# Performance work log

Hardware: AMD Instinct MI355X
Metric: run time of the kernel (lower is better)

The kernel has to match this reference:

```python
import jax, jax.numpy as jnp
import numpy as np

HEADS = 20  # head_dim = 1280 // 20 = 64
LORA_SCALE = 1.0


def setup_inputs() -> dict:
    key = jax.random.key(0)
    ks = jax.random.split(key, 16)
    B, S, C, R = 2, 2048, 1280, 4
    w = 0.02  # keep activations numerically tame
    inp = {
        "x": jax.random.normal(ks[0], (B, S, C), jnp.float32),
        "Wq": jax.random.normal(ks[1], (C, C), jnp.float32) * w,
        "Wk": jax.random.normal(ks[2], (C, C), jnp.float32) * w,
        "Wv": jax.random.normal(ks[3], (C, C), jnp.float32) * w,
        "Wo": jax.random.normal(ks[4], (C, C), jnp.float32) * w,
        "bo": jnp.zeros((C,), jnp.float32),
        "Aq": jax.random.normal(ks[5], (R, C), jnp.float32) * w,
        "Bq": jax.random.normal(ks[6], (C, R), jnp.float32) * w,
        "Ak": jax.random.normal(ks[7], (R, C), jnp.float32) * w,
        "Bk": jax.random.normal(ks[8], (C, R), jnp.float32) * w,
        "Av": jax.random.normal(ks[9], (R, C), jnp.float32) * w,
        "Bv": jax.random.normal(ks[10], (C, R), jnp.float32) * w,
        "Ao": jax.random.normal(ks[11], (R, C), jnp.float32) * w,
        "Bo": jax.random.normal(ks[12], (C, R), jnp.float32) * w,
    }
    return inp


def _lora(x, A, B):
    # LoRALinearLayer: up(down(x)); network_alpha=None -> no extra scaling
    return (x @ A.T) @ B.T


def reference(x, Wq, Wk, Wv, Wo, bo, Aq, Bq, Ak, Bk, Av, Bv, Ao, Bo):
    B, S, C = x.shape
    H = HEADS
    D = C // H
    # base projections + LoRA updates (self-attention: encoder_hidden_states = x)
    q = x @ Wq.T + LORA_SCALE * _lora(x, Aq, Bq)
    k = x @ Wk.T + LORA_SCALE * _lora(x, Ak, Bk)
    v = x @ Wv.T + LORA_SCALE * _lora(x, Av, Bv)
    # head split: [B, S, H, D]
    q = q.reshape(B, S, H, D)
    k = k.reshape(B, S, H, D)
    v = v.reshape(B, S, H, D)
    # explicit scores + softmax (attn.get_attention_scores), scale = 1/sqrt(D)
    scale = 1.0 / jnp.sqrt(jnp.asarray(D, x.dtype))
    scores = jnp.einsum("bshd,bthd->bhst", q, k) * scale  # [B, H, S, S]
    probs = jax.nn.softmax(scores, axis=-1)
    ctx = jnp.einsum("bhst,bthd->bshd", probs, v).reshape(B, S, C)
    # output projection (+bias) + LoRA; dropout is identity at eval
    out = ctx @ Wo.T + bo + LORA_SCALE * _lora(ctx, Ao, Bo)
    return out
```

## Files before the change

kernel.cpp:

```cpp
#include <hip/hip_runtime.h>

#define BATCH 2
#define SEQ   2048
#define CH    1280
#define NH    20
#define HD    64
#define BS    (BATCH*SEQ)
#define RK    4

typedef __attribute__((ext_vector_type(2)))  float floatx2;
typedef __attribute__((ext_vector_type(4)))  short bf16x4;
typedef __attribute__((ext_vector_type(8)))  short bf16x8;
typedef __attribute__((ext_vector_type(16))) float floatx16;

__device__ __forceinline__ floatx16 mfma32(bf16x8 a, bf16x8 b, floatx16 c) {
    return __builtin_amdgcn_mfma_f32_32x32x16_bf16(a, b, c, 0, 0, 0);
}

__device__ __forceinline__ unsigned short f2bf(float f) {
    unsigned int u = __float_as_uint(f);
    u += 0x7fffu + ((u >> 16) & 1u);
    return (unsigned short)(u >> 16);
}
__device__ __forceinline__ unsigned int packbf(float hi, float lo) {
    unsigned int a = __float_as_uint(hi) + 0x8000u;
    unsigned int b = __float_as_uint(lo) + 0x8000u;
    return __builtin_amdgcn_perm(a, b, 0x07060302u);
}
__device__ __forceinline__ unsigned int cvtpk(float lo, float hi) {
    unsigned int r;
    asm("v_cvt_pk_bf16_f32 %0, %1, %2" : "=v"(r) : "v"(lo), "v"(hi));
    return r;
}
__device__ __forceinline__ float fexp2(float x) {
#if __has_builtin(__builtin_amdgcn_exp2f)
    return __builtin_amdgcn_exp2f(x);
#else
    return exp2f(x);
#endif
}

__device__ __forceinline__ void cp16(const unsigned short* g, unsigned short* l) {
    __builtin_amdgcn_global_load_lds(
        (const __attribute__((address_space(1))) unsigned int*)g,
        (__attribute__((address_space(3))) unsigned int*)l, 16, 0, 0);
}

#define F4_BLOCKS   (CH * CH / 1024)
#define CAST_BLOCKS (BS * CH / 1024)

__global__ __launch_bounds__(256) void prep(
    const float* __restrict__ x,
    const float* __restrict__ Wq, const float* __restrict__ Wk,
    const float* __restrict__ Wv, const float* __restrict__ Wo,
    const float* __restrict__ Aq, const float* __restrict__ Bq,
    const float* __restrict__ Ak, const float* __restrict__ Bk,
    const float* __restrict__ Av, const float* __restrict__ Bv,
    const float* __restrict__ Ao, const float* __restrict__ Bo,
    unsigned short* __restrict__ wq_bf, unsigned short* __restrict__ wk_bf,
    unsigned short* __restrict__ wv_bf, unsigned short* __restrict__ wo_bf,
    unsigned short* __restrict__ xb)
{
    const int bx = blockIdx.x;
    if (bx < 4 * F4_BLOCKS) {
        int which = bx / F4_BLOCKS;
        int e = ((bx % F4_BLOCKS) * 256 + threadIdx.x) * 4;
        int i = e / CH, j = e % CH;
        const float *W, *A, *Bm;
        unsigned short* o;
        if (which == 0)      { W = Wq; A = Aq; Bm = Bq; o = wq_bf; }
        else if (which == 1) { W = Wk; A = Ak; Bm = Bk; o = wk_bf; }
        else if (which == 2) { W = Wv; A = Av; Bm = Bv; o = wv_bf; }
        else                 { W = Wo; A = Ao; Bm = Bo; o = wo_bf; }
        float4 acc = *(const float4*)(W + e);
#pragma unroll
        for (int r = 0; r < RK; r++) {
            float bm = Bm[i * RK + r];
            float4 a4 = *(const float4*)(A + r * CH + j);
            acc.x += bm * a4.x; acc.y += bm * a4.y;
            acc.z += bm * a4.z; acc.w += bm * a4.w;
        }
        ushort4 ov;
        ov.x = f2bf(acc.x); ov.y = f2bf(acc.y);
        ov.z = f2bf(acc.z); ov.w = f2bf(acc.w);
        *(ushort4*)(o + e) = ov;
    } else {
        int idx = ((bx - 4 * F4_BLOCKS) * 256 + threadIdx.x) * 4;
        float4 v = *(const float4*)(x + idx);
        ushort4 o;
        o.x = f2bf(v.x); o.y = f2bf(v.y); o.z = f2bf(v.z); o.w = f2bf(v.w);
        *(ushort4*)(xb + idx) = o;
    }
}

__device__ __forceinline__ void gemm128(
    const unsigned short* __restrict__ A, const unsigned short* __restrict__ B,
    unsigned short* __restrict__ obf, float oscale, int mode,
    unsigned short* __restrict__ vt)
{
    __shared__ __align__(16) unsigned short smem[2 * 128 * 64];
    unsigned short* sa = smem;
    unsigned short* sb = smem + 128 * 64;
    const int tid = threadIdx.x;
    const int wav = tid >> 6, lane = tid & 63;
    const int n32 = lane & 31, half = lane >> 5;
    const int wr = wav >> 1, wc = wav & 1;

    const int wg  = blockIdx.x + gridDim.x * blockIdx.y;
    const int swz = (wg & 7) * 40 + (wg >> 3);
    const int M0 = (swz / 10) * 128, N0 = (swz % 10) * 128;

    const int rowt = tid >> 3, cct = (tid & 7) ^ (rowt & 7);
    const unsigned short* gA = A + (size_t)(M0 + rowt) * CH + cct * 8;
    const unsigned short* gB = B + (size_t)(N0 + rowt) * CH + cct * 8;

    const int arow0 = wr * 64 + n32, brow0 = wc * 64 + n32;

    floatx16 acc[2][2];
#pragma unroll
    for (int mt = 0; mt < 2; mt++)
#pragma unroll
        for (int nt = 0; nt < 2; nt++)
#pragma unroll
            for (int r = 0; r < 16; r++) acc[mt][nt][r] = 0.f;

    for (int k0 = 0; k0 < CH; k0 += 64) {
#pragma unroll
        for (int g = 0; g < 4; g++) {
            cp16(gA + (size_t)g * 32 * CH, sa + g * 2048 + wav * 512);
            cp16(gB + (size_t)g * 32 * CH, sb + g * 2048 + wav * 512);
        }
        gA += 64; gB += 64;
        __syncthreads();

        bf16x8 av[2][4], bv[2][4];
#pragma unroll
        for (int mt = 0; mt < 2; mt++) {
            const int ar = arow0 + mt * 32, br = brow0 + mt * 32;
#pragma unroll
            for (int ks = 0; ks < 4; ks++) {
                const int cc = ks * 2 + half;
                av[mt][ks] = *(const bf16x8*)(sa + ar * 64 + ((cc ^ (ar & 7)) << 3));
                bv[mt][ks] = *(const bf16x8*)(sb + br * 64 + ((cc ^ (br & 7)) << 3));
            }
        }
#pragma unroll
        for (int ks = 0; ks < 4; ks++)
#pragma unroll
            for (int mt = 0; mt < 2; mt++)
#pragma unroll
                for (int nt = 0; nt < 2; nt++)
                    acc[mt][nt] = mfma32(av[mt][ks], bv[nt][ks], acc[mt][nt]);
        __syncthreads();
    }

    if (mode == 2) {
#pragma unroll
        for (int mt = 0; mt < 2; mt++) {
#pragma unroll
            for (int nt = 0; nt < 2; nt++) {
                const int dl = wc * 64 + nt * 32 + n32;
#pragma unroll
                for (int j = 0; j < 4; j++) {
                    const int u = wr * 16 + mt * 8 + 2 * j + half;
                    uint2 w;
                    w.x = packbf(acc[mt][nt][4 * j + 1], acc[mt][nt][4 * j + 0]);
                    w.y = packbf(acc[mt][nt][4 * j + 3], acc[mt][nt][4 * j + 2]);
                    *(uint2*)(smem + dl * 128 + ((u ^ n32) << 2)) = w;
                }
            }
        }
        __syncthreads();
        const int b = M0 >> 11;
        const int s_in = M0 & (SEQ - 1);
#pragma unroll
        for (int g = 0; g < 8; g++) {
            int cid = g * 256 + tid;
            int dl = cid >> 4, pc = cid & 15;
            int g32 = pc >> 2, p = (pc & 3) >> 1, hb = pc & 1;
            int u1 = 8 * g32 + 4 * p + 2 * hb;
            int sw = dl & 31;
            uint2 r1 = *(const uint2*)(smem + dl * 128 + ((u1 ^ sw) << 2));
            uint2 r2 = *(const uint2*)(smem + dl * 128 + (((u1 + 1) ^ sw) << 2));
            int ch = N0 + dl, h = ch >> 6, d = ch & 63;
            uint4 val; val.x = r1.x; val.y = r1.y; val.z = r2.x; val.w = r2.y;
            *(uint4*)(vt + (size_t)((b * NH + h) * HD + d) * SEQ + s_in + pc * 8) = val;
        }
        return;
    }

#pragma unroll
    for (int mt = 0; mt < 2; mt++) {
#pragma unroll
        for (int nt = 0; nt < 2; nt++) {
            const int col = N0 + wc * 64 + nt * 32 + n32;
#pragma unroll
            for (int r = 0; r < 16; r++) {
                size_t row = (size_t)(M0 + wr * 64 + mt * 32 +
                                      (r & 3) + 8 * (r >> 2) + 4 * half);
                obf[row * CH + col] = f2bf(acc[mt][nt][r] * oscale);
            }
        }
    }
}

__global__ __launch_bounds__(256) void gemm_qkv(
    const unsigned short* __restrict__ xb,
    const unsigned short* __restrict__ wq, const unsigned short* __restrict__ wk,
    const unsigned short* __restrict__ wv,
    unsigned short* __restrict__ q, unsigned short* __restrict__ k,
    unsigned short* __restrict__ vt)
{
    const unsigned short* w = blockIdx.z == 0 ? wq : blockIdx.z == 1 ? wk : wv;
    unsigned short* o = blockIdx.z == 0 ? q : k;
    float scale = blockIdx.z == 0 ? 0.18033688011112042f : 1.0f;
    int mode = blockIdx.z == 2 ? 2 : 0;
    gemm128(xb, w, o, scale, mode, vt);
}

__global__ __launch_bounds__(256) void gemm_o64(
    const unsigned short* __restrict__ A, const unsigned short* __restrict__ B,
    const float* __restrict__ bias, float* __restrict__ out)
{
    __shared__ __align__(16) unsigned short smem[64 * 64 + 128 * 64];
    unsigned short* sa = smem;
    unsigned short* sb = smem + 64 * 64;
    const int tid = threadIdx.x;
    const int wav = tid >> 6, lane = tid & 63;
    const int n32 = lane & 31, half = lane >> 5;

    const int wg  = blockIdx.x;
    const int swz = (wg & 7) * 80 + (wg >> 3);
    const int M0 = (swz / 10) * 64, N0 = (swz % 10) * 128;

    const int rowt = tid >> 3, cct = (tid & 7) ^ (rowt & 7);
    const unsigned short* gA = A + (size_t)(M0 + rowt) * CH + cct * 8;
    const unsigned short* gB = B + (size_t)(N0 + rowt) * CH + cct * 8;

    const int brow = wav * 32 + n32;

    floatx16 acc[2];
#pragma unroll
    for (int mt = 0; mt < 2; mt++)
#pragma unroll
        for (int r = 0; r < 16; r++) acc[mt][r] = 0.f;

    for (int k0 = 0; k0 < CH; k0 += 64) {
#pragma unroll
        for (int g = 0; g < 2; g++)
            cp16(gA + (size_t)g * 32 * CH, sa + g * 2048 + wav * 512);
#pragma unroll
        for (int g = 0; g < 4; g++)
            cp16(gB + (size_t)g * 32 * CH, sb + g * 2048 + wav * 512);
        gA += 64; gB += 64;
        __syncthreads();

        bf16x8 av[2][4], bv[4];
#pragma unroll
        for (int ks = 0; ks < 4; ks++) {
            const int cc = ks * 2 + half;
#pragma unroll
            for (int mt = 0; mt < 2; mt++) {
                const int ar = mt * 32 + n32;
                av[mt][ks] = *(const bf16x8*)(sa + ar * 64 + ((cc ^ (ar & 7)) << 3));
            }
            bv[ks] = *(const bf16x8*)(sb + brow * 64 + ((cc ^ (brow & 7)) << 3));
        }
#pragma unroll
        for (int ks = 0; ks < 4; ks++)
#pragma unroll
            for (int mt = 0; mt < 2; mt++)
                acc[mt] = mfma32(av[mt][ks], bv[ks], acc[mt]);
        __syncthreads();
    }

    const int col = N0 + wav * 32 + n32;
    const float bv2 = bias[col];
#pragma unroll
    for (int mt = 0; mt < 2; mt++) {
#pragma unroll
        for (int r = 0; r < 16; r++) {
            size_t row = (size_t)(M0 + mt * 32 + (r & 3) + 8 * (r >> 2) + 4 * half);
            out[row * CH + col] = acc[mt][r] + bv2;
        }
    }
}

__global__ __launch_bounds__(512, 4) void attention(
    const unsigned short* __restrict__ q, const unsigned short* __restrict__ k,
    const unsigned short* __restrict__ vt, unsigned short* __restrict__ c_bf)
{
    __shared__ __align__(16) unsigned short smem[2 * (128 * 64 + 64 * 128)];

    const int tid = threadIdx.x, wav = tid >> 6, lane = tid & 63;
    const int n32 = lane & 31, half = lane >> 5;
    const int qg = wav >> 1, kh = wav & 1;

    const int wg  = blockIdx.x + gridDim.x * blockIdx.y;
    const int swz = (wg & 7) * 80 + (wg >> 3);
    const int q0 = (swz & 15) * 128;
    const int bh = swz >> 4, b = bh / NH, h = bh % NH;

    const size_t qrow = (size_t)(b * SEQ + q0 + qg * 32 + n32);
    bf16x8 qf[4];
#pragma unroll
    for (int f = 0; f < 4; f++)
        qf[f] = *(const bf16x8*)(q + qrow * CH + h * HD + f * 16 + half * 8);

    const int rowk = tid >> 3, cck = (tid & 7) ^ (rowk & 7);
    const int rowv = tid >> 4, ccv = (tid & 15) ^ (rowv & 15);
    const unsigned short* gk0 = k + (size_t)(b * SEQ + rowk) * CH + h * HD + cck * 8;
    const unsigned short* gv0 = vt + (size_t)(bh * HD + rowv) * SEQ + ccv * 8;

    auto STAGE = [&](int t, int bufb) {
        const unsigned short* gk = gk0 + (size_t)t * 128 * CH;
        const unsigned short* gv = gv0 + t * 128;
        unsigned short* lk = smem + bufb * 16384 + wav * 512;
        unsigned short* lv = smem + bufb * 16384 + 8192 + wav * 512;
#pragma unroll
        for (int g = 0; g < 2; g++) {
            cp16(gk + (size_t)g * 64 * CH, lk + g * 4096);
            cp16(gv + (size_t)g * 32 * SEQ, lv + g * 4096);
        }
    };

    floatx2 ps = {0.f, 0.f};
    floatx16 acc[2];
#pragma unroll
    for (int dt = 0; dt < 2; dt++)
#pragma unroll
        for (int r = 0; r < 16; r++) acc[dt][r] = 0.f;

    auto COMPUTE = [&](int bufb) {
        const unsigned short* k_lds = smem + bufb * 16384;
        const unsigned short* v_lds = k_lds + 8192;
#pragma unroll
        for (int ktl = 0; ktl < 2; ktl++) {
            const int kt = kh * 2 + ktl;
            const int keyrow = kt * 32 + n32;
            const unsigned short* kr = k_lds + keyrow * 64;
            floatx16 st;
#pragma unroll
            for (int r = 0; r < 16; r++) st[r] = 0.f;
#pragma unroll
            for (int f = 0; f < 4; f++) {
                int phys = (2 * f + half) ^ (keyrow & 7);
                bf16x8 kf = *(const bf16x8*)(kr + phys * 8);
                st = mfma32(kf, qf[f], st);
            }

#pragma unroll
            for (int pp = 0; pp < 2; pp++) {
                float p[8];
#pragma unroll
                for (int r = 0; r < 8; r++) p[r] = fexp2(st[8 * pp + r]);
#pragma unroll
                for (int j = 0; j < 4; j++)
                    ps += (floatx2){p[2 * j], p[2 * j + 1]};
                unsigned int lo0 = cvtpk(p[0], p[1]);
                unsigned int lo1 = cvtpk(p[2], p[3]);
                unsigned int hi0 = cvtpk(p[4], p[5]);
                unsigned int hi1 = cvtpk(p[6], p[7]);
                asm volatile("v_permlane32_swap_b32 %0, %1"
                             : "+v"(lo0), "+v"(hi0));
                asm volatile("v_permlane32_swap_b32 %0, %1"
                             : "+v"(lo1), "+v"(hi1));
                union { unsigned int u[4]; bf16x8 v; } pb;
                pb.u[0] = lo0; pb.u[1] = lo1; pb.u[2] = hi0; pb.u[3] = hi1;
                const int ct = kt * 4 + pp * 2 + half;
#pragma unroll
                for (int dt = 0; dt < 2; dt++) {
                    const int drow = dt * 32 + n32;
                    int phys = ct ^ (drow & 15);
                    bf16x8 vv = *(const bf16x8*)(v_lds + drow * 128 + phys * 8);
                    acc[dt] = mfma32(vv, pb.v, acc[dt]);
                }
            }
        }
    };

    STAGE(0, 0);
    for (int it = 0; it < 15; it++) {
        STAGE(it + 1, (it + 1) & 1);
        asm volatile("s_waitcnt vmcnt(4)" ::: "memory");
        __builtin_amdgcn_s_barrier();
        __builtin_amdgcn_sched_barrier(0);
        COMPUTE(it & 1);
        __builtin_amdgcn_s_barrier();
    }
    asm volatile("s_waitcnt vmcnt(0)" ::: "memory");
    __builtin_amdgcn_s_barrier();
    __builtin_amdgcn_sched_barrier(0);
    COMPUTE(1);

    float psum = ps.x + ps.y;
    float* ex = (float*)smem;
#pragma unroll
    for (int p2 = 0; p2 < 2; p2++) {
        __syncthreads();
        if (kh == 1 && (qg >> 1) == p2) {
            float* dst = ex + (size_t)((qg & 1) * 64 + lane) * 33;
#pragma unroll
            for (int dt = 0; dt < 2; dt++)
#pragma unroll
                for (int r = 0; r < 16; r++) dst[dt * 16 + r] = acc[dt][r];
            dst[32] = psum;
        }
        __syncthreads();
        if (kh == 0 && (qg >> 1) == p2) {
            const float* src = ex + (size_t)((qg & 1) * 64 + lane) * 33;
#pragma unroll
            for (int dt = 0; dt < 2; dt++)
#pragma unroll
                for (int r = 0; r < 16; r++) acc[dt][r] += src[dt * 16 + r];
            psum += src[32];
        }
    }
    if (kh) return;

    float tot = psum + __shfl_xor(psum, 32, 64);
    float rinv = __frcp_rn(tot);
    const size_t obase = qrow * CH + h * HD;
#pragma unroll
    for (int dt = 0; dt < 2; dt++) {
#pragma unroll
        for (int jj = 0; jj < 4; jj++) {
            int d = dt * 32 + 8 * jj + 4 * half;
            uint2 o2;
            o2.x = packbf(acc[dt][4 * jj + 1] * rinv, acc[dt][4 * jj + 0] * rinv);
            o2.y = packbf(acc[dt][4 * jj + 3] * rinv, acc[dt][4 * jj + 2] * rinv);
            *(uint2*)(c_bf + obase + d) = o2;
        }
    }
}

extern "C" void kernel_launch(void* const* d_in, const int* in_sizes, int n_in,
                              void* d_out, int out_size, void* d_ws, size_t ws_size,
                              hipStream_t stream)
{
    const float* x  = (const float*)d_in[0];
    const float* Wq = (const float*)d_in[1];
    const float* Wk = (const float*)d_in[2];
    const float* Wv = (const float*)d_in[3];
    const float* Wo = (const float*)d_in[4];
    const float* bo = (const float*)d_in[5];
    const float* Aq = (const float*)d_in[6];
    const float* Bq = (const float*)d_in[7];
    const float* Ak = (const float*)d_in[8];
    const float* Bk = (const float*)d_in[9];
    const float* Av = (const float*)d_in[10];
    const float* Bv = (const float*)d_in[11];
    const float* Ao = (const float*)d_in[12];
    const float* Bo = (const float*)d_in[13];
    float* out = (float*)d_out;

    char* ws = (char*)d_ws;
    size_t off = 0;
    auto alloc = [&](size_t bytes) -> void* {
        void* p = ws + off; off += (bytes + 255) & ~(size_t)255; return p;
    };
    const size_t WB = (size_t)CH * CH, XB = (size_t)BS * CH;
    unsigned short* wq_bf = (unsigned short*)alloc(WB * 2);
    unsigned short* wk_bf = (unsigned short*)alloc(WB * 2);
    unsigned short* wv_bf = (unsigned short*)alloc(WB * 2);
    unsigned short* wo_bf = (unsigned short*)alloc(WB * 2);
    unsigned short* x_bf  = (unsigned short*)alloc(XB * 2);
    unsigned short* q_bf  = (unsigned short*)alloc(XB * 2);
    unsigned short* k_bf  = (unsigned short*)alloc(XB * 2);
    unsigned short* vt_bf = (unsigned short*)alloc(XB * 2);
    unsigned short* c_bf  = (unsigned short*)alloc(XB * 2);
    (void)ws_size; (void)n_in; (void)in_sizes; (void)out_size;

    prep<<<dim3(4 * F4_BLOCKS + CAST_BLOCKS), 256, 0, stream>>>(
        x, Wq, Wk, Wv, Wo, Aq, Bq, Ak, Bk, Av, Bv, Ao, Bo,
        wq_bf, wk_bf, wv_bf, wo_bf, x_bf);

    gemm_qkv<<<dim3(CH / 128, BS / 128, 3), 256, 0, stream>>>(
        x_bf, wq_bf, wk_bf, wv_bf, q_bf, k_bf, vt_bf);

    attention<<<dim3(SEQ / 128, BATCH * NH), 512, 0, stream>>>(
        q_bf, k_bf, vt_bf, c_bf);

    gemm_o64<<<dim3((BS / 64) * (CH / 128)), 256, 0, stream>>>(
        c_bf, wo_bf, bo, out);
}
```

Measured before the change: 242.2 us.

## Double-buffer LDS in projection GEMM to overlap global loads with MFMA

Doubles the shared-memory tile buffer in the 128x128 GEMM so the next K-tile's async global-to-LDS copies are issued before computing the current tile. Uses explicit vmcnt waits and raw barriers so only the previous stage has to land before compute starts. This hides load latency behind MFMA work, at the cost of twice the LDS (64 KB), which may reduce occupancy. The epilogue's reuse of smem must still be safe after the final barrier.

```diff
diff --git a/kernel.cpp b/kernel.cpp
--- a/kernel.cpp
+++ b/kernel.cpp
@@ -98,9 +98,7 @@
     unsigned short* __restrict__ obf, float oscale, int mode,
     unsigned short* __restrict__ vt)
 {
-    __shared__ __align__(16) unsigned short smem[2 * 128 * 64];
-    unsigned short* sa = smem;
-    unsigned short* sb = smem + 128 * 64;
+    __shared__ __align__(16) unsigned short smem[2 * 16384];
     const int tid = threadIdx.x;
     const int wav = tid >> 6, lane = tid & 63;
     const int n32 = lane & 31, half = lane >> 5;
@@ -114,6 +112,18 @@
     const unsigned short* gA = A + (size_t)(M0 + rowt) * CH + cct * 8;
     const unsigned short* gB = B + (size_t)(N0 + rowt) * CH + cct * 8;
 
+    auto STAGE = [&](int t, int bufb) {
+        const unsigned short* gAt = gA + (size_t)t * 64;
+        const unsigned short* gBt = gB + (size_t)t * 64;
+        unsigned short* sa_b = smem + bufb * 16384;
+        unsigned short* sb_b = sa_b + 8192;
+#pragma unroll
+        for (int g = 0; g < 4; g++) {
+            cp16(gAt + (size_t)g * 32 * CH, sa_b + g * 2048 + wav * 512);
+            cp16(gBt + (size_t)g * 32 * CH, sb_b + g * 2048 + wav * 512);
+        }
+    };
+
     const int arow0 = wr * 64 + n32, brow0 = wc * 64 + n32;
 
     floatx16 acc[2][2];
@@ -124,15 +134,9 @@
 #pragma unroll
             for (int r = 0; r < 16; r++) acc[mt][nt][r] = 0.f;
 
-    for (int k0 = 0; k0 < CH; k0 += 64) {
-#pragma unroll
-        for (int g = 0; g < 4; g++) {
-            cp16(gA + (size_t)g * 32 * CH, sa + g * 2048 + wav * 512);
-            cp16(gB + (size_t)g * 32 * CH, sb + g * 2048 + wav * 512);
-        }
-        gA += 64; gB += 64;
-        __syncthreads();
-
+    auto COMPUTE = [&](int bufb) {
+        const unsigned short* sa = smem + bufb * 16384;
+        const unsigned short* sb = sa + 8192;
         bf16x8 av[2][4], bv[2][4];
 #pragma unroll
         for (int mt = 0; mt < 2; mt++) {
@@ -151,8 +155,21 @@
 #pragma unroll
                 for (int nt = 0; nt < 2; nt++)
                     acc[mt][nt] = mfma32(av[mt][ks], bv[nt][ks], acc[mt][nt]);
-        __syncthreads();
-    }
+    };
+
+    STAGE(0, 0);
+    for (int t = 0; t < 19; t++) {
+        STAGE(t + 1, (t + 1) & 1);
+        asm volatile("s_waitcnt vmcnt(8)" ::: "memory");
+        __builtin_amdgcn_s_barrier();
+        __builtin_amdgcn_sched_barrier(0);
+        COMPUTE(t & 1);
+        __builtin_amdgcn_s_barrier();
+    }
+    asm volatile("s_waitcnt vmcnt(0)" ::: "memory");
+    __builtin_amdgcn_s_barrier();
+    __builtin_amdgcn_sched_barrier(0);
+    COMPUTE(1);
 
     if (mode == 2) {
 #pragma unroll
```

After: 242.0 us. No clear change (-0.1%).
